# Kernel optimization log

Hardware: AMD Instinct MI355X
Metric: run time of the kernel (lower is better)

## Reference

```python
import jax, jax.numpy as jnp
import numpy as np

EPS = 1e-6  # torch F.pairwise_distance default eps (added to the elementwise difference)
XI = 1.2


def _pdist(A, B):
    # dist[i, j] = || B[j] - A[i] + EPS ||_2  == || (B[j]+EPS) - A[i] ||_2
    Bp = B + EPS
    sq = (jnp.sum(Bp * Bp, axis=-1)[None, :]
          + jnp.sum(A * A, axis=-1)[:, None]
          - 2.0 * A @ Bp.T)
    return jnp.sqrt(jnp.maximum(sq, 0.0))


def _half_loss(D, M):
    # D: [B, B] distances, row i = anchor. M: [B, B] float same-label mask.
    same_max = jnp.max(D * M, axis=1)                      # max over same-label distances
    diff = D * (1.0 - M)                                   # zero at same-label slots
    diff_max = jnp.max(diff, axis=1)
    # replace same-label slots with diff_max so min picks the smallest diff-label distance
    diff_min = jnp.min(M * diff_max[:, None] + diff, axis=1)
    l = same_max - diff_min + XI
    return jnp.sum(jax.nn.relu(l))


def setup_inputs() -> dict:
    key = jax.random.key(0)
    k1, k2, k3 = jax.random.split(key, 3)
    B, d = 4096, 1024
    v_f = jax.random.normal(k1, (B, d), dtype=jnp.float32)
    i_f = jax.random.normal(k2, (B, d), dtype=jnp.float32)
    y = jax.random.randint(k3, (B,), 0, 64, dtype=jnp.int64)
    return {"v_f": v_f, "i_f": i_f, "y": y}


def reference(v_f, i_f, y):
    M = (y[:, None] == y[None, :]).astype(v_f.dtype)
    # loop 1: anchor i_f[i] vs all v_f  -> D1[i, j] = ||v_f[j] - i_f[i] + eps||
    loss_i = _half_loss(_pdist(i_f, v_f), M)
    # loop 2: anchor v_f[i] vs all i_f  -> D2[i, j] = ||i_f[j] - v_f[i] + eps||
    loss_v = _half_loss(_pdist(v_f, i_f), M)
    return loss_i + loss_v
```

## Files before the change

kernel.cpp:

```cpp
#include <hip/hip_runtime.h>
#include <hip/hip_bf16.h>
#include <hip/hip_fp8.h>


#define MDIM 4096
#define KDIM 1024
#define NT   16

typedef __attribute__((ext_vector_type(16))) float f32x16;
typedef __attribute__((ext_vector_type(8)))  int   i32x8;
typedef __attribute__((ext_vector_type(4)))  int   i32x4;

__device__ __forceinline__ void gload16(const void* g, void* l) {
  __builtin_amdgcn_global_load_lds(
      (const __attribute__((address_space(1))) void*)g,
      (__attribute__((address_space(3))) void*)l,
      16, 0, 0);
}

__device__ __forceinline__ unsigned char f2e4m3(float x) {
  __hip_fp8_e4m3 q(x);
  return (unsigned char)q.__x;
}

#define BAR() do { asm volatile("" ::: "memory"); \
                   __builtin_amdgcn_s_barrier();  \
                   asm volatile("" ::: "memory"); } while (0)

__global__ __launch_bounds__(256) void prep_kernel(
    const float* __restrict__ vf, const float* __restrict__ iff,
    unsigned char* __restrict__ vb8, unsigned char* __restrict__ ib8,
    float* __restrict__ ni, float* __restrict__ nvp,
    int* __restrict__ same_sq, int* __restrict__ diff_sq,
    float* __restrict__ out) {
  const int wid = blockIdx.x * 4 + (threadIdx.x >> 6);
  const int lane = threadIdx.x & 63;
  const int mat = wid >> 12;
  const int row = wid & 4095;
  const float* X = mat ? iff : vf;
  unsigned char* Xb = mat ? ib8 : vb8;

  const float4* xr4 = (const float4*)(X + (size_t)row * KDIM);
  uchar4* xb4 = (uchar4*)(Xb + (size_t)row * KDIM);

  float s = 0.0f;
#pragma unroll
  for (int it = 0; it < 4; ++it) {
    const int idx = it * 64 + lane;
    float4 v = xr4[idx];
    if (mat) {
      s += v.x * v.x + v.y * v.y + v.z * v.z + v.w * v.w;
    } else {
      float ex = v.x + 1e-6f, ey = v.y + 1e-6f, ez = v.z + 1e-6f, ew = v.w + 1e-6f;
      s += ex * ex + ey * ey + ez * ez + ew * ew;
    }
    uchar4 o;
    o.x = f2e4m3(v.x); o.y = f2e4m3(v.y); o.z = f2e4m3(v.z); o.w = f2e4m3(v.w);
    xb4[idx] = o;
  }
  for (int off = 32; off; off >>= 1) s += __shfl_down(s, off);
  if (lane == 0) {
    if (mat) ni[row] = s; else nvp[row] = s;
  }

  const int gi = blockIdx.x * 256 + threadIdx.x;
  if (gi < 2 * MDIM) {
    same_sq[gi] = 0;
    diff_sq[gi] = 0x7F800000;
  }
  if (gi == 0) out[0] = 0.0f;
}

__global__ __launch_bounds__(512, 4) void tri_gemm(
    const unsigned char* __restrict__ vb8, const unsigned char* __restrict__ ib8,
    const float* __restrict__ ni, const float* __restrict__ nvp,
    const int* __restrict__ y,
    int* __restrict__ same_sq, int* __restrict__ diff_sq) {
  __shared__ unsigned char Abuf[2][256][64];
  __shared__ unsigned char Bbuf[2][128][64];
  __shared__ int   yrow[256], ycol[128];
  __shared__ float nAr[256], nBc[128];

  const unsigned char* Amat = ib8;
  const unsigned char* Bmat = vb8;

  const int row0 = blockIdx.y * 256;
  const int col0 = blockIdx.x * 128;

  const int t = threadIdx.x;
  const int w = t >> 6, lane = t & 63;
  const int l32 = lane & 31, hi = lane >> 5;
  const int wr = w >> 1, wc = w & 1;

  auto swz = [](int row) { return (row & 3) ^ ((row >> 2) & 3); };

  auto stageA = [&](unsigned char (&buf)[256][64], int h, int k0s) {
    const int row = h * 128 + (t >> 2);
    const int cD = t & 3;
    const unsigned char* src =
        Amat + (size_t)(row0 + row) * KDIM + k0s + ((cD ^ swz(row)) << 4);
    gload16(src, &buf[h * 128 + (w << 4)][0]);
  };
  auto stageB = [&](unsigned char (&buf)[128][64], int k0s) {
    const int row = t >> 2;
    const int cD = t & 3;
    const unsigned char* src =
        Bmat + (size_t)(col0 + row) * KDIM + k0s + ((cD ^ swz(row)) << 4);
    gload16(src, &buf[w << 4][0]);
  };
  auto ldA = [&](int c, int R) -> i32x8 {
    const int row = wr * 64 + R * 32 + l32;
    const int s = swz(row);
    const i32x4 lo = *(const i32x4*)&Abuf[c][row][((2 * hi) ^ s) << 4];
    const i32x4 hi4 = *(const i32x4*)&Abuf[c][row][((2 * hi + 1) ^ s) << 4];
    i32x8 r;
    r[0] = lo[0]; r[1] = lo[1]; r[2] = lo[2]; r[3] = lo[3];
    r[4] = hi4[0]; r[5] = hi4[1]; r[6] = hi4[2]; r[7] = hi4[3];
    return r;
  };
  auto ldB = [&](int c, int Cb) -> i32x8 {
    const int col = wc * 64 + Cb * 32 + l32;
    const int s = swz(col);
    const i32x4 lo = *(const i32x4*)&Bbuf[c][col][((2 * hi) ^ s) << 4];
    const i32x4 hi4 = *(const i32x4*)&Bbuf[c][col][((2 * hi + 1) ^ s) << 4];
    i32x8 r;
    r[0] = lo[0]; r[1] = lo[1]; r[2] = lo[2]; r[3] = lo[3];
    r[4] = hi4[0]; r[5] = hi4[1]; r[6] = hi4[2]; r[7] = hi4[3];
    return r;
  };

  stageA(Abuf[0], 0, 0);
  stageA(Abuf[0], 1, 0);
  stageB(Bbuf[0], 0);
  stageA(Abuf[1], 0, 64);
  stageA(Abuf[1], 1, 64);
  stageB(Bbuf[1], 64);
  if (t < 256) {
    yrow[t] = y[row0 + t];
    nAr[t] = ni[row0 + t];
  } else if (t < 384) {
    const int c = t - 256;
    ycol[c] = y[col0 + c];
    nBc[c] = nvp[col0 + c];
  }
  asm volatile("s_waitcnt vmcnt(3) lgkmcnt(0)" ::: "memory");
  BAR();

  f32x16 acc[2][2] = {};
  i32x8 aF[2], bFa, bFb;

#define DO_TILE(C, K2)                                                         \
  do {                                                                         \
    aF[0] = ldA(C, 0);                                                         \
    aF[1] = ldA(C, 1);                                                         \
    bFa = ldB(C, 0);                                                           \
    bFb = ldB(C, 1);                                                           \
    BAR();                                                                     \
    stageA(Abuf[C], 0, (K2));                                                  \
    stageA(Abuf[C], 1, (K2));                                                  \
    stageB(Bbuf[C], (K2));                                                     \
    __builtin_amdgcn_s_setprio(1);                                             \
    acc[0][0] = __builtin_amdgcn_mfma_scale_f32_32x32x64_f8f6f4(               \
        aF[0], bFa, acc[0][0], 0, 0, 0, 0x7F7F7F7F, 0, 0x7F7F7F7F);            \
    acc[1][0] = __builtin_amdgcn_mfma_scale_f32_32x32x64_f8f6f4(               \
        aF[1], bFa, acc[1][0], 0, 0, 0, 0x7F7F7F7F, 0, 0x7F7F7F7F);            \
    acc[0][1] = __builtin_amdgcn_mfma_scale_f32_32x32x64_f8f6f4(               \
        aF[0], bFb, acc[0][1], 0, 0, 0, 0x7F7F7F7F, 0, 0x7F7F7F7F);            \
    acc[1][1] = __builtin_amdgcn_mfma_scale_f32_32x32x64_f8f6f4(               \
        aF[1], bFb, acc[1][1], 0, 0, 0, 0x7F7F7F7F, 0, 0x7F7F7F7F);            \
    __builtin_amdgcn_s_setprio(0);                                             \
    asm volatile("s_waitcnt vmcnt(3)" ::: "memory");                           \
    BAR();                                                                     \
  } while (0)

  for (int kt = 0; kt < NT; kt += 2) {
    const int kb = ((kt + 2) & (NT - 1)) * 64;
    const int kc = ((kt + 3) & (NT - 1)) * 64;
    DO_TILE(0, kb);
    DO_TILE(1, kc);
  }
#undef DO_TILE
  asm volatile("s_waitcnt vmcnt(0)" ::: "memory");

  const int rbase0 = row0;
  const int rbase1 = MDIM + col0;
  const float INF = __int_as_float(0x7F800000);

  float cs[2] = {0.0f, 0.0f};
  float cd[2] = {INF, INF};

#pragma unroll
  for (int R = 0; R < 2; ++R) {
#pragma unroll
    for (int g = 0; g < 16; ++g) {
      const int row_loc = wr * 64 + R * 32 + (g & 3) + 8 * (g >> 2) + 4 * hi;
      const float na = nAr[row_loc];
      const int yl = yrow[row_loc];
      float smax = 0.0f;
      float dmin = INF;
#pragma unroll
      for (int Cb = 0; Cb < 2; ++Cb) {
        const int col_loc = wc * 64 + Cb * 32 + l32;
        const float sq = fmaxf(na + nBc[col_loc] - 2.0f * acc[R][Cb][g], 0.0f);
        if (ycol[col_loc] == yl) {
          smax = fmaxf(smax, sq);
          cs[Cb] = fmaxf(cs[Cb], sq);
        } else {
          dmin = fminf(dmin, sq);
          cd[Cb] = fminf(cd[Cb], sq);
        }
      }
#pragma unroll
      for (int off = 1; off < 32; off <<= 1) {
        smax = fmaxf(smax, __shfl_xor(smax, off));
        dmin = fminf(dmin, __shfl_xor(dmin, off));
      }
      if (l32 == g) {
        atomicMax(&same_sq[rbase0 + row_loc], __float_as_int(smax));
        atomicMin(&diff_sq[rbase0 + row_loc], __float_as_int(dmin));
      }
    }
  }
#pragma unroll
  for (int Cb = 0; Cb < 2; ++Cb) {
    float s = cs[Cb], d = cd[Cb];
    s = fmaxf(s, __shfl_xor(s, 32));
    d = fminf(d, __shfl_xor(d, 32));
    if (hi == 0) {
      const int col_loc = wc * 64 + Cb * 32 + l32;
      atomicMax(&same_sq[rbase1 + col_loc], __float_as_int(s));
      atomicMin(&diff_sq[rbase1 + col_loc], __float_as_int(d));
    }
  }
}

__global__ __launch_bounds__(256) void finalize_kernel(
    const int* __restrict__ same_sq, const int* __restrict__ diff_sq,
    float* __restrict__ out) {
  const int i = blockIdx.x * 256 + threadIdx.x;
  const float sm = sqrtf(__int_as_float(same_sq[i]));
  const float dm = sqrtf(__int_as_float(diff_sq[i]));
  float l = fmaxf(sm - dm + 1.2f, 0.0f);
  for (int off = 32; off; off >>= 1) l += __shfl_down(l, off);
  __shared__ float part[4];
  const int w = threadIdx.x >> 6, lane = threadIdx.x & 63;
  if (lane == 0) part[w] = l;
  __syncthreads();
  if (threadIdx.x == 0) atomicAdd(out, part[0] + part[1] + part[2] + part[3]);
}

extern "C" void kernel_launch(void* const* d_in, const int* in_sizes, int n_in,
                              void* d_out, int out_size, void* d_ws, size_t ws_size,
                              hipStream_t stream) {
  const float* vf = (const float*)d_in[0];
  const float* iff = (const float*)d_in[1];
  const int* y = (const int*)d_in[2];
  float* out = (float*)d_out;

  char* ws = (char*)d_ws;
  unsigned char* vb8 = (unsigned char*)ws;
  unsigned char* ib8 = (unsigned char*)(ws + (4u << 20));
  float* nv  = (float*)(ws + (8u << 20));
  float* ni  = nv + 4096;
  float* nvp = nv + 2 * 4096;
  int* same_sq = (int*)(nv + 4 * 4096);
  int* diff_sq = same_sq + 2 * 4096;

  prep_kernel<<<2048, 256, 0, stream>>>(vf, iff, vb8, ib8, ni, nvp,
                                        same_sq, diff_sq, out);
  tri_gemm<<<dim3(32, 16), 512, 0, stream>>>(vb8, ib8, ni, nvp, y,
                                             same_sq, diff_sq);
  finalize_kernel<<<32, 256, 0, stream>>>(same_sq, diff_sq, out);
}
```

Measured before the change: 60.00 us.

## Drop LDS staging in fp8 GEMM; load MFMA operands directly from global

Replaces the double-buffered LDS pipeline (global_load_lds staging, swizzled LDS reads, barriers) with direct per-lane global vector loads feeding the MFMA instructions. The block tile shrinks from 256x128 with 512 threads to 128x128 with 256 threads, and the grid doubles to 32x32 blocks. The aim is to remove barrier and LDS traffic overhead and rely on L2 and cache reuse instead. The cost is more global and L2 traffic per block, no explicit prefetch overlap, and strided 32-byte per-lane loads that may coalesce poorly.

```diff
diff --git a/kernel.cpp b/kernel.cpp
--- a/kernel.cpp
+++ b/kernel.cpp
@@ -9,23 +9,11 @@
 
 typedef __attribute__((ext_vector_type(16))) float f32x16;
 typedef __attribute__((ext_vector_type(8)))  int   i32x8;
-typedef __attribute__((ext_vector_type(4)))  int   i32x4;
-
-__device__ __forceinline__ void gload16(const void* g, void* l) {
-  __builtin_amdgcn_global_load_lds(
-      (const __attribute__((address_space(1))) void*)g,
-      (__attribute__((address_space(3))) void*)l,
-      16, 0, 0);
-}
 
 __device__ __forceinline__ unsigned char f2e4m3(float x) {
   __hip_fp8_e4m3 q(x);
   return (unsigned char)q.__x;
 }
-
-#define BAR() do { asm volatile("" ::: "memory"); \
-                   __builtin_amdgcn_s_barrier();  \
-                   asm volatile("" ::: "memory"); } while (0)
 
 __global__ __launch_bounds__(256) void prep_kernel(
     const float* __restrict__ vf, const float* __restrict__ iff,
@@ -71,20 +59,15 @@
   if (gi == 0) out[0] = 0.0f;
 }
 
-__global__ __launch_bounds__(512, 4) void tri_gemm(
+__global__ __launch_bounds__(256, 2) void tri_gemm(
     const unsigned char* __restrict__ vb8, const unsigned char* __restrict__ ib8,
     const float* __restrict__ ni, const float* __restrict__ nvp,
     const int* __restrict__ y,
     int* __restrict__ same_sq, int* __restrict__ diff_sq) {
-  __shared__ unsigned char Abuf[2][256][64];
-  __shared__ unsigned char Bbuf[2][128][64];
-  __shared__ int   yrow[256], ycol[128];
-  __shared__ float nAr[256], nBc[128];
-
-  const unsigned char* Amat = ib8;
-  const unsigned char* Bmat = vb8;
-
-  const int row0 = blockIdx.y * 256;
+  __shared__ int   yrow[128], ycol[128];
+  __shared__ float nAr[128], nBc[128];
+
+  const int row0 = blockIdx.y * 128;
   const int col0 = blockIdx.x * 128;
 
   const int t = threadIdx.x;
@@ -92,95 +75,41 @@
   const int l32 = lane & 31, hi = lane >> 5;
   const int wr = w >> 1, wc = w & 1;
 
-  auto swz = [](int row) { return (row & 3) ^ ((row >> 2) & 3); };
-
-  auto stageA = [&](unsigned char (&buf)[256][64], int h, int k0s) {
-    const int row = h * 128 + (t >> 2);
-    const int cD = t & 3;
-    const unsigned char* src =
-        Amat + (size_t)(row0 + row) * KDIM + k0s + ((cD ^ swz(row)) << 4);
-    gload16(src, &buf[h * 128 + (w << 4)][0]);
-  };
-  auto stageB = [&](unsigned char (&buf)[128][64], int k0s) {
-    const int row = t >> 2;
-    const int cD = t & 3;
-    const unsigned char* src =
-        Bmat + (size_t)(col0 + row) * KDIM + k0s + ((cD ^ swz(row)) << 4);
-    gload16(src, &buf[w << 4][0]);
-  };
-  auto ldA = [&](int c, int R) -> i32x8 {
-    const int row = wr * 64 + R * 32 + l32;
-    const int s = swz(row);
-    const i32x4 lo = *(const i32x4*)&Abuf[c][row][((2 * hi) ^ s) << 4];
-    const i32x4 hi4 = *(const i32x4*)&Abuf[c][row][((2 * hi + 1) ^ s) << 4];
-    i32x8 r;
-    r[0] = lo[0]; r[1] = lo[1]; r[2] = lo[2]; r[3] = lo[3];
-    r[4] = hi4[0]; r[5] = hi4[1]; r[6] = hi4[2]; r[7] = hi4[3];
-    return r;
-  };
-  auto ldB = [&](int c, int Cb) -> i32x8 {
-    const int col = wc * 64 + Cb * 32 + l32;
-    const int s = swz(col);
-    const i32x4 lo = *(const i32x4*)&Bbuf[c][col][((2 * hi) ^ s) << 4];
-    const i32x4 hi4 = *(const i32x4*)&Bbuf[c][col][((2 * hi + 1) ^ s) << 4];
-    i32x8 r;
-    r[0] = lo[0]; r[1] = lo[1]; r[2] = lo[2]; r[3] = lo[3];
-    r[4] = hi4[0]; r[5] = hi4[1]; r[6] = hi4[2]; r[7] = hi4[3];
-    return r;
-  };
-
-  stageA(Abuf[0], 0, 0);
-  stageA(Abuf[0], 1, 0);
-  stageB(Bbuf[0], 0);
-  stageA(Abuf[1], 0, 64);
-  stageA(Abuf[1], 1, 64);
-  stageB(Bbuf[1], 64);
-  if (t < 256) {
+  if (t < 128) {
     yrow[t] = y[row0 + t];
     nAr[t] = ni[row0 + t];
-  } else if (t < 384) {
-    const int c = t - 256;
+  } else {
+    const int c = t - 128;
     ycol[c] = y[col0 + c];
     nBc[c] = nvp[col0 + c];
   }
-  asm volatile("s_waitcnt vmcnt(3) lgkmcnt(0)" ::: "memory");
-  BAR();
+  __syncthreads();
+
+  const unsigned char* pa0 =
+      ib8 + (size_t)(row0 + wr * 64 + l32) * KDIM + hi * 32;
+  const unsigned char* pa1 = pa0 + 32 * KDIM;
+  const unsigned char* pb0 =
+      vb8 + (size_t)(col0 + wc * 64 + l32) * KDIM + hi * 32;
+  const unsigned char* pb1 = pb0 + 32 * KDIM;
 
   f32x16 acc[2][2] = {};
-  i32x8 aF[2], bFa, bFb;
-
-#define DO_TILE(C, K2)                                                         \
-  do {                                                                         \
-    aF[0] = ldA(C, 0);                                                         \
-    aF[1] = ldA(C, 1);                                                         \
-    bFa = ldB(C, 0);                                                           \
-    bFb = ldB(C, 1);                                                           \
-    BAR();                                                                     \
-    stageA(Abuf[C], 0, (K2));                                                  \
-    stageA(Abuf[C], 1, (K2));                                                  \
-    stageB(Bbuf[C], (K2));                                                     \
-    __builtin_amdgcn_s_setprio(1);                                             \
-    acc[0][0] = __builtin_amdgcn_mfma_scale_f32_32x32x64_f8f6f4(               \
-        aF[0], bFa, acc[0][0], 0, 0, 0, 0x7F7F7F7F, 0, 0x7F7F7F7F);            \
-    acc[1][0] = __builtin_amdgcn_mfma_scale_f32_32x32x64_f8f6f4(               \
-        aF[1], bFa, acc[1][0], 0, 0, 0, 0x7F7F7F7F, 0, 0x7F7F7F7F);            \
-    acc[0][1] = __builtin_amdgcn_mfma_scale_f32_32x32x64_f8f6f4(               \
-        aF[0], bFb, acc[0][1], 0, 0, 0, 0x7F7F7F7F, 0, 0x7F7F7F7F);            \
-    acc[1][1] = __builtin_amdgcn_mfma_scale_f32_32x32x64_f8f6f4(               \
-        aF[1], bFb, acc[1][1], 0, 0, 0, 0x7F7F7F7F, 0, 0x7F7F7F7F);            \
-    __builtin_amdgcn_s_setprio(0);                                             \
-    asm volatile("s_waitcnt vmcnt(3)" ::: "memory");                           \
-    BAR();                                                                     \
-  } while (0)
-
-  for (int kt = 0; kt < NT; kt += 2) {
-    const int kb = ((kt + 2) & (NT - 1)) * 64;
-    const int kc = ((kt + 3) & (NT - 1)) * 64;
-    DO_TILE(0, kb);
-    DO_TILE(1, kc);
-  }
-#undef DO_TILE
-  asm volatile("s_waitcnt vmcnt(0)" ::: "memory");
+
+#pragma unroll
+  for (int kt = 0; kt < NT; ++kt) {
+    const int k0 = kt * 64;
+    i32x8 a0 = *(const i32x8*)(pa0 + k0);
+    i32x8 a1 = *(const i32x8*)(pa1 + k0);
+    i32x8 b0 = *(const i32x8*)(pb0 + k0);
+    i32x8 b1 = *(const i32x8*)(pb1 + k0);
+    acc[0][0] = __builtin_amdgcn_mfma_scale_f32_32x32x64_f8f6f4(
+        a0, b0, acc[0][0], 0, 0, 0, 0x7F7F7F7F, 0, 0x7F7F7F7F);
+    acc[1][0] = __builtin_amdgcn_mfma_scale_f32_32x32x64_f8f6f4(
+        a1, b0, acc[1][0], 0, 0, 0, 0x7F7F7F7F, 0, 0x7F7F7F7F);
+    acc[0][1] = __builtin_amdgcn_mfma_scale_f32_32x32x64_f8f6f4(
+        a0, b1, acc[0][1], 0, 0, 0, 0x7F7F7F7F, 0, 0x7F7F7F7F);
+    acc[1][1] = __builtin_amdgcn_mfma_scale_f32_32x32x64_f8f6f4(
+        a1, b1, acc[1][1], 0, 0, 0, 0x7F7F7F7F, 0, 0x7F7F7F7F);
+  }
 
   const int rbase0 = row0;
   const int rbase1 = MDIM + col0;
@@ -268,7 +197,7 @@
 
   prep_kernel<<<2048, 256, 0, stream>>>(vf, iff, vb8, ib8, ni, nvp,
                                         same_sq, diff_sq, out);
-  tri_gemm<<<dim3(32, 16), 512, 0, stream>>>(vb8, ib8, ni, nvp, y,
+  tri_gemm<<<dim3(32, 32), 256, 0, stream>>>(vb8, ib8, ni, nvp, y,
                                              same_sq, diff_sq);
   finalize_kernel<<<32, 256, 0, stream>>>(same_sq, diff_sq, out);
 }
```

Result: slower. 152.2 us (+153.6%).
